# Optimization experiments

Hardware: AMD Instinct MI355X
Metric: run time of the kernel (lower is better)

The kernel has to match this reference:

```python
import jax, jax.numpy as jnp
import numpy as np

WEIGHT = 1.0


def _smooth_l1(pred, target):
    # F.smooth_l1_loss default: beta=1.0, reduction='mean'
    d = jnp.abs(pred - target)
    loss = jnp.where(d < 1.0, 0.5 * d * d, d - 0.5)
    return jnp.mean(loss)


def setup_inputs() -> dict:
    key = jax.random.key(0)
    k0, k1, k2 = jax.random.split(key, 3)
    B, L = 4096, 128
    return {
        "outputs0": jax.random.normal(k0, (B, B), dtype=jnp.float32),
        "outputs1": jax.random.normal(k1, (B, B), dtype=jnp.float32),
        "labels": jax.random.normal(k2, (B, L), dtype=jnp.float32),
    }


def reference(outputs0, outputs1, labels):
    # vector = [labels | ones]  -> [B, 2L]
    ones = jnp.ones_like(labels)
    vector = jnp.concatenate([labels, ones], axis=1)
    cos1 = vector @ vector.T                                   # [B, B]
    mod = jnp.sqrt(jnp.sum(vector * vector, axis=1, keepdims=True))  # [B, 1]
    cos2 = mod @ mod.T                                         # [B, B]
    multi_labels = jnp.floor(cos1 / cos2)                      # on-device floor (replaces cpu/numpy roundtrip)
    total_loss = (_smooth_l1(outputs0, multi_labels) + _smooth_l1(outputs1, multi_labels)) / 2.0
    return WEIGHT * total_loss
```

## Files before the change

kernel.cpp:

```cpp
#include <hip/hip_runtime.h>
#include <hip/hip_bf16.h>

#define B_N 4096
#define L_K 128
#define NPART 16384

typedef __bf16 bf16x8 __attribute__((ext_vector_type(8)));
typedef float  f32x4  __attribute__((ext_vector_type(4)));

__global__ __launch_bounds__(256) void prep_kernel(const float* __restrict__ labels,
                                                   unsigned short* __restrict__ lb,
                                                   float* __restrict__ inv) {
    const int wave = blockIdx.x * 4 + (threadIdx.x >> 6);
    const int lane = threadIdx.x & 63;
    const int row  = wave;

    const float x0 = labels[row * L_K + lane];
    const float x1 = labels[row * L_K + 64 + lane];

    __hip_bfloat16 h0 = __float2bfloat16(x0);
    __hip_bfloat16 h1 = __float2bfloat16(x1);
    lb[row * L_K + lane]      = *reinterpret_cast<unsigned short*>(&h0);
    lb[row * L_K + 64 + lane] = *reinterpret_cast<unsigned short*>(&h1);

    float s = x0 * x0 + x1 * x1;
    #pragma unroll
    for (int m = 32; m >= 1; m >>= 1) s += __shfl_xor(s, m);
    if (lane == 0) inv[row] = 1.0f / sqrtf(s + 128.0f);
}

__global__ __launch_bounds__(256) void main_kernel(const float* __restrict__ o0,
                                                   const float* __restrict__ o1,
                                                   const unsigned short* __restrict__ lb,
                                                   const float* __restrict__ inv,
                                                   float* __restrict__ partials) {
    __shared__ __align__(16) float m_lds[4][16][68];

    const int w = threadIdx.x >> 6;
    const int l = threadIdx.x & 63;
    const int task = blockIdx.x * 4 + w;
    const int s = task >> 6;
    const int c = task & 63;

    const int fr = l & 15;
    const int fk = (l >> 4) * 8;
    const int g  = l >> 4;
    const int rr = g * 4;
    const int r0 = s * 16;
    const int c0 = c * 64;

    f32x4 p0[4], p1[4];
    #pragma unroll
    for (int v = 0; v < 4; ++v) {
        const size_t goff = (size_t)(r0 + 4 * v + g) * B_N + (size_t)(c0 + fr * 4);
        p0[v] = *reinterpret_cast<const f32x4*>(o0 + goff);
        p1[v] = *reinterpret_cast<const f32x4*>(o1 + goff);
    }

    bf16x8 a[4];
    #pragma unroll
    for (int kk = 0; kk < 4; ++kk)
        a[kk] = *reinterpret_cast<const bf16x8*>(
            lb + (size_t)(r0 + fr) * L_K + kk * 32 + fk);

    f32x4 acc[4] = {};
    #pragma unroll
    for (int kk = 0; kk < 4; ++kk) {
        #pragma unroll
        for (int ct = 0; ct < 4; ++ct) {
            const bf16x8 b = *reinterpret_cast<const bf16x8*>(
                lb + (size_t)(c0 + ct * 16 + fr) * L_K + kk * 32 + fk);
            acc[ct] = __builtin_amdgcn_mfma_f32_16x16x32_bf16(a[kk], b, acc[ct], 0, 0, 0);
        }
    }

    float invi[4];
    #pragma unroll
    for (int r = 0; r < 4; ++r) invi[r] = inv[r0 + rr + r];
    float invj[4];
    #pragma unroll
    for (int ct = 0; ct < 4; ++ct) invj[ct] = inv[c0 + ct * 16 + fr];

    #pragma unroll
    for (int ct = 0; ct < 4; ++ct) {
        #pragma unroll
        for (int r = 0; r < 4; ++r) {
            m_lds[w][rr + r][ct * 16 + fr] =
                floorf((acc[ct][r] + 128.0f) * invi[r] * invj[ct]);
        }
    }

    float sumA = 0.0f, sumB = 0.0f;
    #pragma unroll
    for (int v = 0; v < 4; ++v) {
        const f32x4 mm = *reinterpret_cast<const f32x4*>(&m_lds[w][4 * v + g][fr * 4]);
        #pragma unroll
        for (int q = 0; q < 4; ++q) {
            const float d0 = fabsf(p0[v][q] - mm[q]);
            const float d1 = fabsf(p1[v][q] - mm[q]);
            const float u0 = fminf(d0, 1.0f), v0 = fmaxf(d0, 1.0f);
            const float u1 = fminf(d1, 1.0f), v1 = fmaxf(d1, 1.0f);
            sumA = fmaf(u0, u0, sumA);
            sumA = fmaf(u1, u1, sumA);
            sumB += v0 + v1;
        }
    }

    float lsum = 0.5f * sumA + sumB;
    #pragma unroll
    for (int m = 32; m >= 1; m >>= 1) lsum += __shfl_xor(lsum, m);
    if (l == 0) partials[task] = lsum - 2048.0f;
}

__global__ __launch_bounds__(1024) void fin_kernel(const float* __restrict__ partials,
                                                   float* __restrict__ out) {
    __shared__ double wred[16];
    double s = 0.0;
    for (int i = threadIdx.x; i < NPART; i += 1024) s += (double)partials[i];
    #pragma unroll
    for (int m = 32; m >= 1; m >>= 1) s += __shfl_xor(s, m);
    const int l = threadIdx.x & 63, w = threadIdx.x >> 6;
    if (l == 0) wred[w] = s;
    __syncthreads();
    if (threadIdx.x == 0) {
        double t = 0.0;
        #pragma unroll
        for (int i = 0; i < 16; ++i) t += wred[i];
        out[0] = (float)(t / (2.0 * (double)B_N * (double)B_N));
    }
}

extern "C" void kernel_launch(void* const* d_in, const int* in_sizes, int n_in,
                              void* d_out, int out_size, void* d_ws, size_t ws_size,
                              hipStream_t stream) {
    const float* o0     = (const float*)d_in[0];
    const float* o1     = (const float*)d_in[1];
    const float* labels = (const float*)d_in[2];
    float* out = (float*)d_out;

    char* ws = (char*)d_ws;
    unsigned short* lb = (unsigned short*)ws;
    float* inv      = (float*)(ws + (size_t)B_N * L_K * 2);
    float* partials = (float*)(ws + (size_t)B_N * L_K * 2 + B_N * 4);

    prep_kernel<<<B_N / 4, 256, 0, stream>>>(labels, lb, inv);
    main_kernel<<<NPART / 4, 256, 0, stream>>>(o0, o1, lb, inv, partials);
    fin_kernel<<<1, 1024, 0, stream>>>(partials, out);
}
```

Measured before the change: 169.9 us.

## Split fused gram/loss kernel into byte-packed label matrix and streaming loss pass

Splits the fused kernel into two. A gram kernel writes the floored cosine matrix as one byte per element (offset by one), and a separate streaming loss kernel reads both output matrices together with the byte matrix using fully coalesced, grid-strided vector loads. The goal is to separate MFMA compute from the bandwidth-bound 128 MB read so the loss pass can reach full streaming bandwidth. In exchange it adds a 16 MB write and read of the byte matrix plus an extra launch. It also assumes the label values fit in the range -1 to 254.

```diff
diff --git a/kernel.cpp b/kernel.cpp
--- a/kernel.cpp
+++ b/kernel.cpp
@@ -3,7 +3,9 @@
 
 #define B_N 4096
 #define L_K 128
-#define NPART 16384
+#define NTASK 16384
+#define LOSS_BLOCKS 2048
+#define LOSS_THREADS 524288
 
 typedef __bf16 bf16x8 __attribute__((ext_vector_type(8)));
 typedef float  f32x4  __attribute__((ext_vector_type(4)));
@@ -29,11 +31,9 @@
     if (lane == 0) inv[row] = 1.0f / sqrtf(s + 128.0f);
 }
 
-__global__ __launch_bounds__(256) void main_kernel(const float* __restrict__ o0,
-                                                   const float* __restrict__ o1,
-                                                   const unsigned short* __restrict__ lb,
+__global__ __launch_bounds__(256) void gram_kernel(const unsigned short* __restrict__ lb,
                                                    const float* __restrict__ inv,
-                                                   float* __restrict__ partials) {
+                                                   unsigned char* __restrict__ m8) {
     __shared__ __align__(16) float m_lds[4][16][68];
 
     const int w = threadIdx.x >> 6;
@@ -48,14 +48,6 @@
     const int rr = g * 4;
     const int r0 = s * 16;
     const int c0 = c * 64;
-
-    f32x4 p0[4], p1[4];
-    #pragma unroll
-    for (int v = 0; v < 4; ++v) {
-        const size_t goff = (size_t)(r0 + 4 * v + g) * B_N + (size_t)(c0 + fr * 4);
-        p0[v] = *reinterpret_cast<const f32x4*>(o0 + goff);
-        p1[v] = *reinterpret_cast<const f32x4*>(o1 + goff);
-    }
 
     bf16x8 a[4];
     #pragma unroll
@@ -90,14 +82,39 @@
         }
     }
 
-    float sumA = 0.0f, sumB = 0.0f;
     #pragma unroll
     for (int v = 0; v < 4; ++v) {
         const f32x4 mm = *reinterpret_cast<const f32x4*>(&m_lds[w][4 * v + g][fr * 4]);
+        const unsigned int pk = ((unsigned int)(mm[0] + 1.0f)) |
+                                ((unsigned int)(mm[1] + 1.0f) << 8) |
+                                ((unsigned int)(mm[2] + 1.0f) << 16) |
+                                ((unsigned int)(mm[3] + 1.0f) << 24);
+        const size_t boff = (size_t)(r0 + 4 * v + g) * B_N + (size_t)(c0 + fr * 4);
+        *reinterpret_cast<unsigned int*>(m8 + boff) = pk;
+    }
+}
+
+__global__ __launch_bounds__(256) void loss_kernel(const float* __restrict__ o0,
+                                                   const float* __restrict__ o1,
+                                                   const unsigned char* __restrict__ m8,
+                                                   float* __restrict__ partials) {
+    __shared__ float wsum[4];
+    const int tid = blockIdx.x * 256 + threadIdx.x;
+
+    float sumA = 0.0f, sumB = 0.0f;
+    #pragma unroll
+    for (int k = 0; k < 8; ++k) {
+        const size_t q = (size_t)tid + (size_t)k * LOSS_THREADS;
+        const f32x4 p0 = *reinterpret_cast<const f32x4*>(o0 + q * 4);
+        const f32x4 p1 = *reinterpret_cast<const f32x4*>(o1 + q * 4);
+        const uchar4 mu = *reinterpret_cast<const uchar4*>(m8 + q * 4);
+
+        const float mf[4] = {(float)mu.x - 1.0f, (float)mu.y - 1.0f,
+                             (float)mu.z - 1.0f, (float)mu.w - 1.0f};
         #pragma unroll
-        for (int q = 0; q < 4; ++q) {
-            const float d0 = fabsf(p0[v][q] - mm[q]);
-            const float d1 = fabsf(p1[v][q] - mm[q]);
+        for (int j = 0; j < 4; ++j) {
+            const float d0 = fabsf(p0[j] - mf[j]);
+            const float d1 = fabsf(p1[j] - mf[j]);
             const float u0 = fminf(d0, 1.0f), v0 = fmaxf(d0, 1.0f);
             const float u1 = fminf(d1, 1.0f), v1 = fmaxf(d1, 1.0f);
             sumA = fmaf(u0, u0, sumA);
@@ -106,17 +123,22 @@
         }
     }
 
-    float lsum = 0.5f * sumA + sumB;
+    float lsum = 0.5f * sumA + sumB - 64.0f;
     #pragma unroll
     for (int m = 32; m >= 1; m >>= 1) lsum += __shfl_xor(lsum, m);
-    if (l == 0) partials[task] = lsum - 2048.0f;
+
+    const int w = threadIdx.x >> 6, l = threadIdx.x & 63;
+    if (l == 0) wsum[w] = lsum;
+    __syncthreads();
+    if (threadIdx.x == 0)
+        partials[blockIdx.x] = wsum[0] + wsum[1] + wsum[2] + wsum[3];
 }
 
 __global__ __launch_bounds__(1024) void fin_kernel(const float* __restrict__ partials,
                                                    float* __restrict__ out) {
     __shared__ double wred[16];
     double s = 0.0;
-    for (int i = threadIdx.x; i < NPART; i += 1024) s += (double)partials[i];
+    for (int i = threadIdx.x; i < LOSS_BLOCKS; i += 1024) s += (double)partials[i];
     #pragma unroll
     for (int m = 32; m >= 1; m >>= 1) s += __shfl_xor(s, m);
     const int l = threadIdx.x & 63, w = threadIdx.x >> 6;
@@ -139,11 +161,14 @@
     float* out = (float*)d_out;
 
     char* ws = (char*)d_ws;
+    const size_t MB = 1048576;
     unsigned short* lb = (unsigned short*)ws;
-    float* inv      = (float*)(ws + (size_t)B_N * L_K * 2);
-    float* partials = (float*)(ws + (size_t)B_N * L_K * 2 + B_N * 4);
+    float* inv         = (float*)(ws + MB);
+    float* partials    = (float*)(ws + MB + 16384);
+    unsigned char* m8  = (unsigned char*)(ws + 2 * MB);
 
     prep_kernel<<<B_N / 4, 256, 0, stream>>>(labels, lb, inv);
-    main_kernel<<<NPART / 4, 256, 0, stream>>>(o0, o1, lb, inv, partials);
+    gram_kernel<<<NTASK / 4, 256, 0, stream>>>(lb, inv, m8);
+    loss_kernel<<<LOSS_BLOCKS, 256, 0, stream>>>(o0, o1, m8, partials);
     fin_kernel<<<1, 1024, 0, stream>>>(partials, out);
 }
```

Result: slower. 194.4 us (+14.4%).
